# Performance work log

Measured on AMD Instinct MI355X. Metric: run time of the kernel, lower is better.

The kernel has to match this reference:

```python
import jax, jax.numpy as jnp
import numpy as np

HEAD = 8
LN_EPS = 1e-5


def setup_inputs() -> dict:
    key = jax.random.key(0)
    k1, k2, k3, k4 = jax.random.split(key, 4)
    B, N, C = 1, 4096, 128
    x = jax.random.normal(k1, (B, N, C), dtype=jnp.float32)
    A = jax.random.normal(k2, (B, N, HEAD, 1), dtype=jnp.float32)
    # xavier-ish scaled params
    W_qk = jax.random.normal(k3, (C, 2 * C), dtype=jnp.float32) * (1.0 / np.sqrt(C))
    W_v = jax.random.normal(k4, (1, 1), dtype=jnp.float32)
    ln_g = jnp.ones((C,), dtype=jnp.float32)
    ln_b = jnp.zeros((C,), dtype=jnp.float32)
    return {"x": x, "A": A, "W_qk": W_qk, "W_v": W_v, "ln_g": ln_g, "ln_b": ln_b}


def _layernorm(x, g, b):
    mu = jnp.mean(x, axis=-1, keepdims=True)
    var = jnp.mean(jnp.square(x - mu), axis=-1, keepdims=True)
    return (x - mu) * jax.lax.rsqrt(var + LN_EPS) * g + b


def reference(x, A, W_qk, W_v, ln_g, ln_b):
    B, N, C = x.shape
    hd = C // HEAD
    scale = C ** (-0.5)  # NOTE: full dim, as in original (dim ** -0.5)
    xn = _layernorm(x, ln_g, ln_b)
    qk = (xn @ W_qk).reshape(B, N, 2, HEAD, hd)
    q = jnp.transpose(qk[:, :, 0], (0, 2, 1, 3))  # [B,H,N,hd]
    k = jnp.transpose(qk[:, :, 1], (0, 2, 1, 3))  # [B,H,N,hd]
    v = A * W_v[0, 0]                              # Linear(1,1,bias=False)
    v = jnp.transpose(v, (0, 2, 1, 3))             # [B,H,N,1]
    scores = jnp.einsum("bhnd,bhmd->bhnm", q, k) * scale
    attn = jax.nn.softmax(scores, axis=-1)
    out = jnp.einsum("bhnm,bhmv->bhnv", attn, v)   # [B,H,N,1]
    A_plus = jnp.transpose(out, (0, 2, 1, 3))      # [B,N,H,1]
    return A + A_plus
```

## Files before the change

### kernel.cpp

```cpp
#include <hip/hip_runtime.h>

#define HEADS 8
#define NTOK 4096
#define CH 128
#define KSPLIT 8
#define KCHUNK (NTOK / KSPLIT)
#define LN_EPS 1e-5f

typedef short short8 __attribute__((ext_vector_type(8)));
typedef float f32x4 __attribute__((ext_vector_type(4)));

__device__ inline unsigned short f2bf(float f) {
    unsigned int u = __float_as_uint(f);
    u = (u + 0x7FFFu + ((u >> 16) & 1u)) >> 16;
    return (unsigned short)u;
}

__device__ inline float fast_exp2(float x) {
#if __has_builtin(__builtin_amdgcn_exp2f)
    return __builtin_amdgcn_exp2f(x);
#else
    float r; asm volatile("v_exp_f32 %0, %1" : "=v"(r) : "v"(x)); return r;
#endif
}

#define SC (0.08838834764831845f * 1.4426950408889634f)

__global__ __launch_bounds__(256) void ln_qk_fused(
    const float* __restrict__ x, const float* __restrict__ Wqk,
    const float* __restrict__ g, const float* __restrict__ b,
    unsigned short* __restrict__ qb, unsigned short* __restrict__ kbuf)
{
    __shared__ __align__(16) unsigned short xn_s[16][CH];
    const int tid = threadIdx.x;
    const int wave = tid >> 6, lane = tid & 63;
    const int row0 = blockIdx.x * 16;
    const int ct = blockIdx.y * 4 + wave;
    const int j = lane & 15, grp = lane >> 4;

    const float sc = (ct < 8) ? SC : 1.0f;
    short8 wf[4];
    #pragma unroll
    for (int ks = 0; ks < 4; ++ks) {
        unsigned int uu0, uu1, uu2, uu3;
        const float* wp = Wqk + (ks * 32 + grp * 8) * 256 + ct * 16 + j;
        uu0 = f2bf(wp[0 * 256] * sc) | ((unsigned)f2bf(wp[1 * 256] * sc) << 16);
        uu1 = f2bf(wp[2 * 256] * sc) | ((unsigned)f2bf(wp[3 * 256] * sc) << 16);
        uu2 = f2bf(wp[4 * 256] * sc) | ((unsigned)f2bf(wp[5 * 256] * sc) << 16);
        uu3 = f2bf(wp[6 * 256] * sc) | ((unsigned)f2bf(wp[7 * 256] * sc) << 16);
        uint4 packed = {uu0, uu1, uu2, uu3};
        wf[ks] = *(short8*)&packed;
    }

    for (int rr = wave; rr < 16; rr += 4) {
        const int row = row0 + rr;
        float2 xv = *(const float2*)(x + row * CH + lane * 2);
        float s  = xv.x + xv.y;
        float sq = xv.x * xv.x + xv.y * xv.y;
        #pragma unroll
        for (int off = 32; off >= 1; off >>= 1) {
            s  += __shfl_xor(s, off);
            sq += __shfl_xor(sq, off);
        }
        float mu  = s * (1.0f / CH);
        float var = sq * (1.0f / CH) - mu * mu;
        float rs  = rsqrtf(var + LN_EPS);
        float2 gv = *(const float2*)(g + lane * 2);
        float2 bv = *(const float2*)(b + lane * 2);
        xn_s[rr][lane * 2]     = f2bf((xv.x - mu) * rs * gv.x + bv.x);
        xn_s[rr][lane * 2 + 1] = f2bf((xv.y - mu) * rs * gv.y + bv.y);
    }
    __syncthreads();

    short8 af[4];
    #pragma unroll
    for (int ks = 0; ks < 4; ++ks)
        af[ks] = *(const short8*)(&xn_s[j][ks * 32 + grp * 8]);

    f32x4 acc = {0.f, 0.f, 0.f, 0.f};
    #pragma unroll
    for (int ks = 0; ks < 4; ++ks)
        acc = __builtin_amdgcn_mfma_f32_16x16x32_bf16(af[ks], wf[ks], acc, 0, 0, 0);

    unsigned short* dst = (ct < 8)
        ? qb   + ((size_t)ct * NTOK + row0) * 16
        : kbuf + ((size_t)(ct - 8) * NTOK + row0) * 16;
    #pragma unroll
    for (int r = 0; r < 4; ++r)
        dst[(grp * 4 + r) * 16 + j] = f2bf(acc[r]);
}

__global__ __launch_bounds__(256) void attn_kernel(
    const unsigned short* __restrict__ qb, const unsigned short* __restrict__ kbuf,
    const float* __restrict__ A,
    float* __restrict__ partE, float* __restrict__ partF)
{
    const int tid = threadIdx.x;
    const int wave = tid >> 6, lane = tid & 63;
    const int ksp = blockIdx.y, h = blockIdx.z;
    const int q0 = blockIdx.x * 128 + wave * 32;
    const int m0 = ksp * KCHUNK;
    const int j = lane & 15;
    const int grp = lane >> 4;
    const int kh = grp & 1;

    short8 qf0 = *(const short8*)(qb + ((size_t)(h * NTOK + q0 + j) * 16 + kh * 8));
    short8 qf1 = *(const short8*)(qb + ((size_t)(h * NTOK + q0 + 16 + j) * 16 + kh * 8));
    if (lane >= 32) { qf0 = (short8)0; qf1 = (short8)0; }

    const unsigned short* kbase = kbuf + ((size_t)h * NTOK + m0) * 16;
    const float* abase = A + (size_t)(m0 + grp * 4) * HEADS + h;

    float E0 = 0.f, F0 = 0.f, E1 = 0.f, F1 = 0.f;

    short8 kf = *(const short8*)(kbase + (j * 16 + kh * 8));
    float v0 = abase[0 * HEADS], v1 = abase[1 * HEADS];
    float v2 = abase[2 * HEADS], v3 = abase[3 * HEADS];

    for (int mi = 0; mi < KCHUNK; mi += 16) {
        const int nx = (mi + 16 < KCHUNK) ? mi + 16 : 0;
        short8 kn = *(const short8*)(kbase + ((nx + j) * 16 + kh * 8));
        float n0 = abase[(nx + 0) * HEADS], n1 = abase[(nx + 1) * HEADS];
        float n2 = abase[(nx + 2) * HEADS], n3 = abase[(nx + 3) * HEADS];

        f32x4 z = {0.f, 0.f, 0.f, 0.f};
        f32x4 s0 = __builtin_amdgcn_mfma_f32_16x16x32_bf16(kf, qf0, z, 0, 0, 0);
        f32x4 s1 = __builtin_amdgcn_mfma_f32_16x16x32_bf16(kf, qf1, z, 0, 0, 0);

        #pragma unroll
        for (int r = 0; r < 4; ++r) {
            float vr = (r == 0) ? v0 : (r == 1) ? v1 : (r == 2) ? v2 : v3;
            float p0 = fast_exp2(s0[r]);
            float p1 = fast_exp2(s1[r]);
            E0 += p0; F0 = fmaf(p0, vr, F0);
            E1 += p1; F1 = fmaf(p1, vr, F1);
        }
        kf = kn; v0 = n0; v1 = n1; v2 = n2; v3 = n3;
    }

    #pragma unroll
    for (int off = 16; off < 64; off <<= 1) {
        E0 += __shfl_xor(E0, off);
        F0 += __shfl_xor(F0, off);
        E1 += __shfl_xor(E1, off);
        F1 += __shfl_xor(F1, off);
    }

    if (lane < 16) {
        const int base = (ksp * HEADS + h) * NTOK;
        partE[base + q0 + j]      = E0;
        partF[base + q0 + j]      = F0;
        partE[base + q0 + 16 + j] = E1;
        partF[base + q0 + 16 + j] = F1;
    }
}

__global__ __launch_bounds__(256) void reduce_kernel(
    const float* __restrict__ partE, const float* __restrict__ partF,
    const float* __restrict__ A, const float* __restrict__ Wv,
    float* __restrict__ out)
{
    const int t = blockIdx.x * 256 + threadIdx.x;
    const int n = t >> 3;
    const int h = t & 7;
    float E = 0.f, F = 0.f;
    #pragma unroll
    for (int s = 0; s < KSPLIT; ++s) {
        E += partE[(s * HEADS + h) * NTOK + n];
        F += partF[(s * HEADS + h) * NTOK + n];
    }
    out[t] = A[t] + Wv[0] * F / E;
}

extern "C" void kernel_launch(void* const* d_in, const int* in_sizes, int n_in,
                              void* d_out, int out_size, void* d_ws, size_t ws_size,
                              hipStream_t stream)
{
    const float* x   = (const float*)d_in[0];
    const float* A   = (const float*)d_in[1];
    const float* Wqk = (const float*)d_in[2];
    const float* Wv  = (const float*)d_in[3];
    const float* g   = (const float*)d_in[4];
    const float* b   = (const float*)d_in[5];
    float* out = (float*)d_out;

    float* partE = (float*)d_ws;
    float* partF = partE + KSPLIT * HEADS * NTOK;
    unsigned short* qb   = (unsigned short*)(partF + KSPLIT * HEADS * NTOK);
    unsigned short* kbuf = qb + (size_t)HEADS * NTOK * 16;

    ln_qk_fused<<<dim3(NTOK / 16, 4), dim3(256), 0, stream>>>(x, Wqk, g, b, qb, kbuf);
    attn_kernel<<<dim3(NTOK / 128, KSPLIT, HEADS), dim3(256), 0, stream>>>(
        qb, kbuf, A, partE, partF);
    reduce_kernel<<<dim3(NTOK * HEADS / 256), dim3(256), 0, stream>>>(
        partE, partF, A, Wv, out);
}
```

Before: 36.77 us.

## Transpose V, use 16x16x16 MFMA, swizzle LDS, and pack exp accumulation

The LN/QK kernel now also writes a head-major transposed copy of A (vT). Each of its blocks handles 32 rows, and the LDS tile uses an XOR swizzle with 32-bit stores. The attention kernel swaps the half-zeroed 16x16x32 MFMA for the K=16 variant with 4-element fragments. It reads V as one float4 per lane from vT instead of four strided gathers, and accumulates with packed 2-wide FMAs in a loop unrolled by 4. The goal is less wasted MFMA work and lower load and ALU overhead in the inner loop. The trade-offs are an extra transposed buffer write and a prefetch that reads past the end of each chunk into adjacent workspace.

Result: slower. 39.26 us (+6.8%).

```diff
diff --git a/kernel.cpp b/kernel.cpp
--- a/kernel.cpp
+++ b/kernel.cpp
@@ -5,10 +5,13 @@
 #define CH 128
 #define KSPLIT 8
 #define KCHUNK (NTOK / KSPLIT)
+#define ROWS 32
 #define LN_EPS 1e-5f
 
 typedef short short8 __attribute__((ext_vector_type(8)));
+typedef short short4v __attribute__((ext_vector_type(4)));
 typedef float f32x4 __attribute__((ext_vector_type(4)));
+typedef float f32x2 __attribute__((ext_vector_type(2)));
 
 __device__ inline unsigned short f2bf(float f) {
     unsigned int u = __float_as_uint(f);
@@ -24,17 +27,39 @@
 #endif
 }
 
+__device__ inline f32x2 fma2(f32x2 a, f32x2 b, f32x2 c) {
+#if __has_builtin(__builtin_elementwise_fma)
+    return __builtin_elementwise_fma(a, b, c);
+#else
+    f32x2 r; r.x = fmaf(a.x, b.x, c.x); r.y = fmaf(a.y, b.y, c.y); return r;
+#endif
+}
+
+__device__ inline f32x4 mfma16(short4v a, short4v b, f32x4 c) {
+#if __has_builtin(__builtin_amdgcn_mfma_f32_16x16x16bf16_1k)
+    return __builtin_amdgcn_mfma_f32_16x16x16bf16_1k(a, b, c, 0, 0, 0);
+#elif __has_builtin(__builtin_amdgcn_mfma_f32_16x16x16_bf16)
+    return __builtin_amdgcn_mfma_f32_16x16x16_bf16(a, b, c, 0, 0, 0);
+#else
+    short8 a8 = {a.x, a.y, a.z, a.w, (short)0, (short)0, (short)0, (short)0};
+    short8 b8 = {b.x, b.y, b.z, b.w, (short)0, (short)0, (short)0, (short)0};
+    return __builtin_amdgcn_mfma_f32_16x16x32_bf16(a8, b8, c, 0, 0, 0);
+#endif
+}
+
 #define SC (0.08838834764831845f * 1.4426950408889634f)
 
 __global__ __launch_bounds__(256) void ln_qk_fused(
     const float* __restrict__ x, const float* __restrict__ Wqk,
     const float* __restrict__ g, const float* __restrict__ b,
-    unsigned short* __restrict__ qb, unsigned short* __restrict__ kbuf)
-{
-    __shared__ __align__(16) unsigned short xn_s[16][CH];
+    const float* __restrict__ A,
+    unsigned short* __restrict__ qb, unsigned short* __restrict__ kbuf,
+    float* __restrict__ vT)
+{
+    __shared__ __align__(16) unsigned short xn_s[ROWS][CH];
     const int tid = threadIdx.x;
     const int wave = tid >> 6, lane = tid & 63;
-    const int row0 = blockIdx.x * 16;
+    const int row0 = blockIdx.x * ROWS;
     const int ct = blockIdx.y * 4 + wave;
     const int j = lane & 15, grp = lane >> 4;
 
@@ -52,7 +77,12 @@
         wf[ks] = *(short8*)&packed;
     }
 
-    for (int rr = wave; rr < 16; rr += 4) {
+    if (blockIdx.y == 0) {
+        const int hh = tid >> 5, r = tid & 31;
+        vT[hh * NTOK + row0 + r] = A[(size_t)(row0 + r) * HEADS + hh];
+    }
+
+    for (int rr = wave; rr < ROWS; rr += 4) {
         const int row = row0 + rr;
         float2 xv = *(const float2*)(x + row * CH + lane * 2);
         float s  = xv.x + xv.y;
@@ -67,32 +97,38 @@
         float rs  = rsqrtf(var + LN_EPS);
         float2 gv = *(const float2*)(g + lane * 2);
         float2 bv = *(const float2*)(b + lane * 2);
-        xn_s[rr][lane * 2]     = f2bf((xv.x - mu) * rs * gv.x + bv.x);
-        xn_s[rr][lane * 2 + 1] = f2bf((xv.y - mu) * rs * gv.y + bv.y);
+        unsigned int lo = f2bf((xv.x - mu) * rs * gv.x + bv.x);
+        unsigned int hi = f2bf((xv.y - mu) * rs * gv.y + bv.y);
+        const int c = (lane * 2) ^ ((rr & 7) << 3);
+        *(unsigned int*)&xn_s[rr][c] = lo | (hi << 16);
     }
     __syncthreads();
 
-    short8 af[4];
-    #pragma unroll
-    for (int ks = 0; ks < 4; ++ks)
-        af[ks] = *(const short8*)(&xn_s[j][ks * 32 + grp * 8]);
-
-    f32x4 acc = {0.f, 0.f, 0.f, 0.f};
-    #pragma unroll
-    for (int ks = 0; ks < 4; ++ks)
-        acc = __builtin_amdgcn_mfma_f32_16x16x32_bf16(af[ks], wf[ks], acc, 0, 0, 0);
-
-    unsigned short* dst = (ct < 8)
-        ? qb   + ((size_t)ct * NTOK + row0) * 16
-        : kbuf + ((size_t)(ct - 8) * NTOK + row0) * 16;
-    #pragma unroll
-    for (int r = 0; r < 4; ++r)
-        dst[(grp * 4 + r) * 16 + j] = f2bf(acc[r]);
+    #pragma unroll
+    for (int t = 0; t < 2; ++t) {
+        short8 af[4];
+        #pragma unroll
+        for (int ks = 0; ks < 4; ++ks)
+            af[ks] = *(const short8*)(&xn_s[t * 16 + j]
+                                          [(ks * 32 + grp * 8) ^ ((j & 7) << 3)]);
+
+        f32x4 acc = {0.f, 0.f, 0.f, 0.f};
+        #pragma unroll
+        for (int ks = 0; ks < 4; ++ks)
+            acc = __builtin_amdgcn_mfma_f32_16x16x32_bf16(af[ks], wf[ks], acc, 0, 0, 0);
+
+        unsigned short* dst = (ct < 8)
+            ? qb   + ((size_t)ct * NTOK + row0 + t * 16) * 16
+            : kbuf + ((size_t)(ct - 8) * NTOK + row0 + t * 16) * 16;
+        #pragma unroll
+        for (int r = 0; r < 4; ++r)
+            dst[(grp * 4 + r) * 16 + j] = f2bf(acc[r]);
+    }
 }
 
 __global__ __launch_bounds__(256) void attn_kernel(
     const unsigned short* __restrict__ qb, const unsigned short* __restrict__ kbuf,
-    const float* __restrict__ A,
+    const float* __restrict__ vT,
     float* __restrict__ partE, float* __restrict__ partF)
 {
     const int tid = threadIdx.x;
@@ -100,58 +136,62 @@
     const int ksp = blockIdx.y, h = blockIdx.z;
     const int q0 = blockIdx.x * 128 + wave * 32;
     const int m0 = ksp * KCHUNK;
-    const int j = lane & 15;
-    const int grp = lane >> 4;
-    const int kh = grp & 1;
-
-    short8 qf0 = *(const short8*)(qb + ((size_t)(h * NTOK + q0 + j) * 16 + kh * 8));
-    short8 qf1 = *(const short8*)(qb + ((size_t)(h * NTOK + q0 + 16 + j) * 16 + kh * 8));
-    if (lane >= 32) { qf0 = (short8)0; qf1 = (short8)0; }
-
-    const unsigned short* kbase = kbuf + ((size_t)h * NTOK + m0) * 16;
-    const float* abase = A + (size_t)(m0 + grp * 4) * HEADS + h;
-
-    float E0 = 0.f, F0 = 0.f, E1 = 0.f, F1 = 0.f;
-
-    short8 kf = *(const short8*)(kbase + (j * 16 + kh * 8));
-    float v0 = abase[0 * HEADS], v1 = abase[1 * HEADS];
-    float v2 = abase[2 * HEADS], v3 = abase[3 * HEADS];
-
+    const int j = lane & 15, grp = lane >> 4;
+
+    short4v qf0 = *(const short4v*)(qb + ((size_t)(h * NTOK + q0 + j) * 16 + grp * 4));
+    short4v qf1 = *(const short4v*)(qb + ((size_t)(h * NTOK + q0 + 16 + j) * 16 + grp * 4));
+
+    const unsigned short* kl = kbuf + ((size_t)(h * NTOK + m0 + j) * 16 + grp * 4);
+    const float* vl = vT + h * NTOK + m0 + grp * 4;
+
+    f32x2 E0 = {0.f, 0.f}, F0 = {0.f, 0.f};
+    f32x2 E1 = {0.f, 0.f}, F1 = {0.f, 0.f};
+
+    short4v kf = *(const short4v*)kl;
+    f32x4 vv = *(const f32x4*)vl;
+
+    #pragma unroll 4
     for (int mi = 0; mi < KCHUNK; mi += 16) {
-        const int nx = (mi + 16 < KCHUNK) ? mi + 16 : 0;
-        short8 kn = *(const short8*)(kbase + ((nx + j) * 16 + kh * 8));
-        float n0 = abase[(nx + 0) * HEADS], n1 = abase[(nx + 1) * HEADS];
-        float n2 = abase[(nx + 2) * HEADS], n3 = abase[(nx + 3) * HEADS];
+        short4v kn = *(const short4v*)(kl + (size_t)(mi + 16) * 16);
+        f32x4 vn = *(const f32x4*)(vl + mi + 16);
 
         f32x4 z = {0.f, 0.f, 0.f, 0.f};
-        f32x4 s0 = __builtin_amdgcn_mfma_f32_16x16x32_bf16(kf, qf0, z, 0, 0, 0);
-        f32x4 s1 = __builtin_amdgcn_mfma_f32_16x16x32_bf16(kf, qf1, z, 0, 0, 0);
-
-        #pragma unroll
-        for (int r = 0; r < 4; ++r) {
-            float vr = (r == 0) ? v0 : (r == 1) ? v1 : (r == 2) ? v2 : v3;
-            float p0 = fast_exp2(s0[r]);
-            float p1 = fast_exp2(s1[r]);
-            E0 += p0; F0 = fmaf(p0, vr, F0);
-            E1 += p1; F1 = fmaf(p1, vr, F1);
-        }
-        kf = kn; v0 = n0; v1 = n1; v2 = n2; v3 = n3;
-    }
+        f32x4 s0 = mfma16(kf, qf0, z);
+        f32x4 s1 = mfma16(kf, qf1, z);
+
+        f32x2 p01, p23, r01, r23;
+        p01.x = fast_exp2(s0[0]); p01.y = fast_exp2(s0[1]);
+        p23.x = fast_exp2(s0[2]); p23.y = fast_exp2(s0[3]);
+        r01.x = fast_exp2(s1[0]); r01.y = fast_exp2(s1[1]);
+        r23.x = fast_exp2(s1[2]); r23.y = fast_exp2(s1[3]);
+
+        E0 += p01 + p23;
+        F0 = fma2(p01, vv.xy, F0);
+        F0 = fma2(p23, vv.zw, F0);
+        E1 += r01 + r23;
+        F1 = fma2(r01, vv.xy, F1);
+        F1 = fma2(r23, vv.zw, F1);
+
+        kf = kn; vv = vn;
+    }
+
+    float e0 = E0.x + E0.y, f0 = F0.x + F0.y;
+    float e1 = E1.x + E1.y, f1 = F1.x + F1.y;
 
     #pragma unroll
     for (int off = 16; off < 64; off <<= 1) {
-        E0 += __shfl_xor(E0, off);
-        F0 += __shfl_xor(F0, off);
-        E1 += __shfl_xor(E1, off);
-        F1 += __shfl_xor(F1, off);
+        e0 += __shfl_xor(e0, off);
+        f0 += __shfl_xor(f0, off);
+        e1 += __shfl_xor(e1, off);
+        f1 += __shfl_xor(f1, off);
     }
 
     if (lane < 16) {
         const int base = (ksp * HEADS + h) * NTOK;
-        partE[base + q0 + j]      = E0;
-        partF[base + q0 + j]      = F0;
-        partE[base + q0 + 16 + j] = E1;
-        partF[base + q0 + 16 + j] = F1;
+        partE[base + q0 + j]      = e0;
+        partF[base + q0 + j]      = f0;
+        partE[base + q0 + 16 + j] = e1;
+        partF[base + q0 + 16 + j] = f1;
     }
 }
 
@@ -184,14 +224,16 @@
     const float* b   = (const float*)d_in[5];
     float* out = (float*)d_out;
 
-    float* partE = (float*)d_ws;
-    float* partF = partE + KSPLIT * HEADS * NTOK;
-    unsigned short* qb   = (unsigned short*)(partF + KSPLIT * HEADS * NTOK);
+    unsigned short* qb   = (unsigned short*)d_ws;
     unsigned short* kbuf = qb + (size_t)HEADS * NTOK * 16;
-
-    ln_qk_fused<<<dim3(NTOK / 16, 4), dim3(256), 0, stream>>>(x, Wqk, g, b, qb, kbuf);
+    float* vT    = (float*)(kbuf + (size_t)HEADS * NTOK * 16);
+    float* partE = vT + (size_t)HEADS * NTOK;
+    float* partF = partE + (size_t)KSPLIT * HEADS * NTOK;
+
+    ln_qk_fused<<<dim3(NTOK / ROWS, 4), dim3(256), 0, stream>>>(
+        x, Wqk, g, b, A, qb, kbuf, vT);
     attn_kernel<<<dim3(NTOK / 128, KSPLIT, HEADS), dim3(256), 0, stream>>>(
-        qb, kbuf, A, partE, partF);
+        qb, kbuf, vT, partE, partF);
     reduce_kernel<<<dim3(NTOK * HEADS / 256), dim3(256), 0, stream>>>(
         partE, partF, A, Wv, out);
 }
```
